# Kernel tuning notes

Measured on AMD Instinct MI355X. Metric: run time of the kernel, lower is better.

The kernel has to match this reference:

```python
import jax, jax.numpy as jnp
import numpy as np

B, S, E = 4, 1024, 1024
H, DH = 16, 64
P = 64  # prompt length
MASKED_BIAS = -10000.0


def setup_inputs() -> dict:
    key = jax.random.key(0)
    ks = jax.random.split(key, 9)
    return {
        "hidden_states": jax.random.normal(ks[0], (B, S, E), jnp.float32),
        "promptKey": jax.random.normal(ks[1], (B, H, P, DH), jnp.float32),
        "promptValue": jax.random.normal(ks[2], (B, H, P, DH), jnp.float32),
        "textualKey": jax.random.normal(ks[3], (B, H, S, DH), jnp.float32),
        "textualValue": jax.random.normal(ks[4], (B, H, S, DH), jnp.float32),
        "promptMask": jnp.ones((B, 1, S, P), jnp.bool_),
        "c_attn_w": jax.random.normal(ks[5], (E, 3 * E), jnp.float32) * 0.02,
        "c_attn_b": jnp.zeros((3 * E,), jnp.float32),
        "c_proj_w": jax.random.normal(ks[6], (E, E), jnp.float32) * 0.02,
        "c_proj_b": jnp.zeros((E,), jnp.float32),
    }


def _split_heads(t):
    # [B, S, E] -> [B, H, S, DH]
    b, s, _ = t.shape
    return t.reshape(b, s, H, DH).transpose(0, 2, 1, 3)


def reference(hidden_states, promptKey, promptValue, textualKey, textualValue,
              promptMask, c_attn_w, c_attn_b, c_proj_w, c_proj_b):
    qkv = hidden_states @ c_attn_w + c_attn_b          # [B,S,3E]
    q, k, v = jnp.split(qkv, 3, axis=-1)
    q, k, v = _split_heads(q), _split_heads(k), _split_heads(v)  # [B,H,S,DH]

    # scores against prompt KV, textual KV, and elementwise self term
    promptW = jnp.einsum("bhsd,bhpd->bhsp", q, promptKey)       # [B,H,S,P]
    textW = jnp.einsum("bhsd,bhtd->bhst", q, textualKey)        # [B,H,S,S]
    selfW = jnp.sum(q * k, axis=-1, keepdims=True)              # [B,H,S,1]
    attn_weights = jnp.concatenate((promptW, textW, selfW), axis=-1)
    attn_weights = attn_weights / jnp.sqrt(jnp.float32(DH))

    # non-residual causal mask: bias[qlen-qlen:qlen, 1:klen+1] -> strictly lower tri
    causal = jnp.tri(S, S, -1, dtype=bool)                      # [S,S]
    self_mask = jnp.ones((S, 1), dtype=bool)
    causal_self = jnp.concatenate((causal, self_mask), axis=-1)[None, None]  # [1,1,S,S+1]
    full_mask = jnp.concatenate(
        (promptMask, jnp.broadcast_to(causal_self, (B, 1, S, S + 1))), axis=-1)
    attn_weights = jnp.where(full_mask, attn_weights, MASKED_BIAS)
    attn_weights = jax.nn.softmax(attn_weights, axis=-1)

    wSelf = attn_weights[..., -1:]                              # [B,H,S,1]
    wRest = attn_weights[..., :-1]                              # [B,H,S,P+S]
    valuePast = jnp.concatenate((promptValue, textualValue), axis=-2)  # [B,H,P+S,DH]
    attn_output = jnp.einsum("bhsk,bhkd->bhsd", wRest, valuePast) + wSelf * v

    # merge heads and output projection
    attn_output = attn_output.transpose(0, 2, 1, 3).reshape(B, S, E)
    return attn_output @ c_proj_w + c_proj_b
```

## Files before the change

### kernel.cpp

```cpp
#include <hip/hip_runtime.h>
#include <hip/hip_bf16.h>
#include <stdint.h>

#define H_ 16
#define DH_ 64
#define S_ 1024
#define B_ 4
#define E_ 1024
#define P_ 64
#define BH_ (B_ * H_)
#define KV_ (P_ + S_)
#define NT_ 17
#define TILE_ELEMS 4096

typedef __attribute__((ext_vector_type(8))) short short8;
typedef __attribute__((ext_vector_type(4))) float floatx4;

#define MFMA_BF16(a, b, c) __builtin_amdgcn_mfma_f32_16x16x32_bf16((a), (b), (c), 0, 0, 0)

__device__ __forceinline__ float bf2f(unsigned short u) {
    union { float f; uint32_t i; } x;
    x.i = ((uint32_t)u) << 16;
    return x.f;
}
__device__ __forceinline__ unsigned short f2bf(float f) {
    uint32_t i = __float_as_uint(f);
    uint32_t r = (i + 0x7fffu + ((i >> 16) & 1u)) >> 16;
    return (unsigned short)r;
}

__device__ __forceinline__ void gl_lds16(const void* g, void* l) {
    __builtin_amdgcn_global_load_lds(
        (const __attribute__((address_space(1))) uint32_t*)g,
        (__attribute__((address_space(3))) uint32_t*)l, 16, 0, 0);
}

#define BARRIER() asm volatile("s_barrier" ::: "memory")
#define WAIT_VM(n) asm volatile("s_waitcnt vmcnt(" #n ")" ::: "memory")

__global__ void prep(const float* __restrict__ hidden, const float* __restrict__ cw,
                     const float* __restrict__ pw, const float* __restrict__ pK,
                     const float* __restrict__ tK, const float* __restrict__ pV,
                     const float* __restrict__ tV, unsigned short* __restrict__ Ah,
                     unsigned short* __restrict__ Wt1, unsigned short* __restrict__ Wt2,
                     unsigned short* __restrict__ Kp, unsigned short* __restrict__ Vp) {
    __shared__ float t[32][33];
    int bid = blockIdx.x, tid = threadIdx.x;
    if (bid < 4096) {
        int i = bid * 256 + tid;
        float4 v = ((const float4*)hidden)[i];
        ushort4 o;
        o.x = f2bf(v.x); o.y = f2bf(v.y); o.z = f2bf(v.z); o.w = f2bf(v.w);
        ((ushort4*)Ah)[i] = o;
    } else if (bid < 8192) {
        const float* in; unsigned short* out; int R, C, bxx, byy;
        if (bid < 7168) { int i = bid - 4096; in = cw; out = Wt1; R = 1024; C = 3072; bxx = i % 96; byy = i / 96; }
        else            { int i = bid - 7168; in = pw; out = Wt2; R = 1024; C = 1024; bxx = i % 32; byy = i / 32; }
        int tx = tid & 31, ty = tid >> 5;
        int c0 = bxx * 32, r0 = byy * 32;
#pragma unroll
        for (int i = 0; i < 4; ++i)
            t[ty + i * 8][tx] = in[(size_t)(r0 + ty + i * 8) * C + c0 + tx];
        __syncthreads();
#pragma unroll
        for (int i = 0; i < 4; ++i)
            out[(size_t)(c0 + ty + i * 8) * R + r0 + tx] = f2bf(t[tx][ty + i * 8]);
    } else {
        int gid0 = (bid - 8192) * 256 + tid;
        int half = gid0 / (BH_ * 8704);
        int gid = gid0 % (BH_ * 8704);
        int bh = gid / 8704, rem = gid % 8704;
        int tt = rem / 512, r2 = rem % 512;
        int f = r2 >> 6, lane = r2 & 63;
        int nt = f >> 1, h = f & 1, quad = lane >> 4, cl = lane & 15;
        unsigned short o[8];
        if (half == 0) {
            int key = tt * 64 + nt * 16 + cl;
            int dh = h * 32 + quad * 8;
            const float* src = (key < P_)
                ? pK + ((size_t)bh * P_ + key) * DH_ + dh
                : tK + ((size_t)bh * S_ + (key - P_)) * DH_ + dh;
#pragma unroll
            for (int u = 0; u < 8; ++u) o[u] = f2bf(src[u]);
            *(int4*)&Kp[(size_t)gid * 8] = *(int4*)o;
        } else {
            int dhn = nt * 16 + cl;
            int kbase = tt * 64 + h * 32 + quad * 8;
            const float* src = (kbase < P_)
                ? pV + ((size_t)bh * P_ + kbase) * DH_ + dhn
                : tV + ((size_t)bh * S_ + (kbase - P_)) * DH_ + dhn;
#pragma unroll
            for (int u = 0; u < 8; ++u) o[u] = f2bf(src[(size_t)u * DH_]);
            *(int4*)&Vp[(size_t)gid * 8] = *(int4*)o;
        }
    }
}

template <int MODE, int TM, int TN, int BK>
__global__ __launch_bounds__(256) void gemm_bt(
    const unsigned short* __restrict__ A, const unsigned short* __restrict__ Bt,
    const float* __restrict__ bias, float* __restrict__ Cout,
    unsigned short* __restrict__ Qo, unsigned short* __restrict__ Ko,
    unsigned short* __restrict__ Vo, int M, int N, int K) {
    constexpr int MI = TM / 32, NI = TN / 32;
    constexpr int NA = TM * BK / 2048;
    constexpr int NB = TN * BK / 2048;
    static_assert(NA + NB == 4, "vmcnt constant assumes 4 loads/tile");
    __shared__ __align__(16) unsigned short lA[2][TM * BK];
    __shared__ __align__(16) unsigned short lB[2][TN * BK];
    int tid = threadIdx.x;
    int wave = tid >> 6, lane = tid & 63, quad = lane >> 4, cl = lane & 15;
    int m0 = blockIdx.y * TM, n0 = blockIdx.x * TN;
    int wm = (wave >> 1) * (TM / 2), wn = (wave & 1) * (TN / 2);
    floatx4 acc[MI][NI];
#pragma unroll
    for (int mi = 0; mi < MI; ++mi)
#pragma unroll
        for (int ni = 0; ni < NI; ++ni) acc[mi][ni] = (floatx4){0.f, 0.f, 0.f, 0.f};

    auto issue = [&](int k0, int buf) {
#pragma unroll
        for (int li = 0; li < NA; ++li) {
            int o = (li * 256 + tid) * 16;
            int hh = o / (TM * 64), rr = (o % (TM * 64)) >> 6, c8 = (o >> 4) & 3;
            gl_lds16(A + (size_t)(m0 + rr) * K + k0 + hh * 32 + c8 * 8,
                     (char*)lA[buf] + o);
        }
#pragma unroll
        for (int li = 0; li < NB; ++li) {
            int o = (li * 256 + tid) * 16;
            int hh = o / (TN * 64), rr = (o % (TN * 64)) >> 6, c8 = (o >> 4) & 3;
            gl_lds16(Bt + (size_t)(n0 + rr) * K + k0 + hh * 32 + c8 * 8,
                     (char*)lB[buf] + o);
        }
    };
    auto compute = [&](int buf) {
#pragma unroll
        for (int kk = 0; kk < BK / 32; ++kk) {
            short8 af[MI], bfr[NI];
#pragma unroll
            for (int mi = 0; mi < MI; ++mi)
                af[mi] = *(const short8*)&lA[buf][kk * TM * 32 + (wm + mi * 16 + cl) * 32 + quad * 8];
#pragma unroll
            for (int ni = 0; ni < NI; ++ni)
                bfr[ni] = *(const short8*)&lB[buf][kk * TN * 32 + (wn + ni * 16 + cl) * 32 + quad * 8];
#pragma unroll
            for (int mi = 0; mi < MI; ++mi)
#pragma unroll
                for (int ni = 0; ni < NI; ++ni)
                    acc[mi][ni] = MFMA_BF16(af[mi], bfr[ni], acc[mi][ni]);
        }
    };

    int nT = K / BK;
    issue(0, 0);
    for (int t = 0; t < nT; ++t) {
        int buf = t & 1;
        if (t + 1 < nT) {
            issue((t + 1) * BK, buf ^ 1);
            WAIT_VM(4);
        } else {
            WAIT_VM(0);
        }
        BARRIER();
        compute(buf);
        BARRIER();
    }

#pragma unroll
    for (int ni = 0; ni < NI; ++ni) {
        int ncol = n0 + wn + ni * 16 + cl;
        float bv = bias[ncol];
#pragma unroll
        for (int mi = 0; mi < MI; ++mi) {
#pragma unroll
            for (int r = 0; r < 4; ++r) {
                int mrow = m0 + wm + mi * 16 + quad * 4 + r;
                float v = acc[mi][ni][r] + bv;
                if (MODE == 0) {
                    Cout[(size_t)mrow * N + ncol] = v;
                } else {
                    int which = ncol >> 10, e = ncol & 1023;
                    int hh = e >> 6, dh = e & 63;
                    int b = mrow >> 10, s = mrow & 1023;
                    size_t idx = ((size_t)(b * H_ + hh) * S_ + s) * DH_ + dh;
                    unsigned short* dst = (which == 0) ? Qo : ((which == 1) ? Ko : Vo);
                    dst[idx] = f2bf(v);
                }
            }
        }
    }
}

__global__ __launch_bounds__(256) void attn_k(
    const unsigned short* __restrict__ Q, const unsigned short* __restrict__ Kc,
    const unsigned short* __restrict__ Vc, const unsigned short* __restrict__ Kp,
    const unsigned short* __restrict__ Vp, unsigned short* __restrict__ Aout) {
    __shared__ __align__(16) unsigned short lP[4][16 * 72];
    int tid = threadIdx.x, wave = tid >> 6, lane = tid & 63;
    int quad = lane >> 4, cl = lane & 15;
    int l = blockIdx.x;
    int p = l >> 6, bh = l & 63;
    int b = bh >> 4, h = bh & 15;
    const unsigned short* Qb = Q + (size_t)bh * S_ * DH_;
    const unsigned short* Kb = Kc + (size_t)bh * S_ * DH_;
    const unsigned short* Vb = Vc + (size_t)bh * S_ * DH_;
    const unsigned short* Kpb = Kp + (size_t)bh * NT_ * TILE_ELEMS;
    const unsigned short* Vpb = Vp + (size_t)bh * NT_ * TILE_ELEMS;
    unsigned short* lp = lP[wave];

    int x1 = p, x2 = 15 - p;
    int qb1 = x1 * 64 + wave * 16, qb2 = x2 * 64 + wave * 16;

    short8 a0_1 = *(const short8*)(Qb + (size_t)(qb1 + cl) * DH_ + quad * 8);
    short8 a1_1 = *(const short8*)(Qb + (size_t)(qb1 + cl) * DH_ + quad * 8 + 32);
    short8 a0_2 = *(const short8*)(Qb + (size_t)(qb2 + cl) * DH_ + quad * 8);
    short8 a1_2 = *(const short8*)(Qb + (size_t)(qb2 + cl) * DH_ + quad * 8 + 32);

    float lsum1[4] = {0.f, 0.f, 0.f, 0.f}, lsum2[4] = {0.f, 0.f, 0.f, 0.f};
    floatx4 O1[4], O2[4];
#pragma unroll
    for (int nt = 0; nt < 4; ++nt) {
        O1[nt] = (floatx4){0.f, 0.f, 0.f, 0.f};
        O2[nt] = (floatx4){0.f, 0.f, 0.f, 0.f};
    }

    int rl = wave * 16 + quad * 4;

    auto do_tile = [&](const unsigned short* Kt, const unsigned short* Vt,
                       short8 a0, short8 a1, floatx4* O, float* lsum, bool diag) {
        floatx4 s[4];
        short8 k0[4], k1[4], v0[4], v1[4];
#pragma unroll
        for (int nt = 0; nt < 4; ++nt) {
            k0[nt] = *(const short8*)&Kt[(nt * 2 + 0) * 512 + lane * 8];
            k1[nt] = *(const short8*)&Kt[(nt * 2 + 1) * 512 + lane * 8];
        }
#pragma unroll
        for (int nt = 0; nt < 4; ++nt) {
            s[nt] = (floatx4){0.f, 0.f, 0.f, 0.f};
            s[nt] = MFMA_BF16(a0, k0[nt], s[nt]);
            s[nt] = MFMA_BF16(a1, k1[nt], s[nt]);
        }
#pragma unroll
        for (int nt = 0; nt < 4; ++nt) {
            v0[nt] = *(const short8*)&Vt[(nt * 2 + 0) * 512 + lane * 8];
            v1[nt] = *(const short8*)&Vt[(nt * 2 + 1) * 512 + lane * 8];
        }
#pragma unroll
        for (int nt = 0; nt < 4; ++nt) {
            int col = nt * 16 + cl;
#pragma unroll
            for (int r = 0; r < 4; ++r) {
                float v = s[nt][r] * 0.125f;
                if (diag && col >= rl + r) v = -10000.0f;
                float pb = __expf(v);
                lsum[r] += pb;
                lp[(quad * 4 + r) * 72 + col] = f2bf(pb);
            }
        }
        asm volatile("s_waitcnt lgkmcnt(0)" ::: "memory");
        short8 p0 = *(const short8*)&lp[cl * 72 + quad * 8];
        short8 p1 = *(const short8*)&lp[cl * 72 + quad * 8 + 32];
#pragma unroll
        for (int nt = 0; nt < 4; ++nt) {
            O[nt] = MFMA_BF16(p0, v0[nt], O[nt]);
            O[nt] = MFMA_BF16(p1, v1[nt], O[nt]);
        }
    };

    int T1 = x1 + 2, Tu = x2 + 2;
    for (int t = 0; t < Tu; ++t) {
        const unsigned short* Kt = Kpb + (size_t)t * TILE_ELEMS;
        const unsigned short* Vt = Vpb + (size_t)t * TILE_ELEMS;
        do_tile(Kt, Vt, a0_2, a1_2, O2, lsum2, t == Tu - 1);
        if (t < T1) do_tile(Kt, Vt, a0_1, a1_1, O1, lsum1, t == T1 - 1);
    }

#pragma unroll
    for (int seg = 0; seg < 2; ++seg) {
        int qb = seg ? qb2 : qb1;
        float* lsum = seg ? lsum2 : lsum1;
        floatx4* O = seg ? O2 : O1;
#pragma unroll
        for (int r = 0; r < 4; ++r) {
            float rs = lsum[r];
            rs += __shfl_xor(rs, 1, 16);
            rs += __shfl_xor(rs, 2, 16);
            rs += __shfl_xor(rs, 4, 16);
            rs += __shfl_xor(rs, 8, 16);
            int row = qb + quad * 4 + r;
            const unsigned short* qp = Qb + (size_t)row * DH_ + cl * 4;
            const unsigned short* kp = Kb + (size_t)row * DH_ + cl * 4;
            float d = 0.f;
#pragma unroll
            for (int u = 0; u < 4; ++u) d += bf2f(qp[u]) * bf2f(kp[u]);
            d += __shfl_xor(d, 1, 16);
            d += __shfl_xor(d, 2, 16);
            d += __shfl_xor(d, 4, 16);
            d += __shfl_xor(d, 8, 16);
            float ps = __expf(d * 0.125f);
            float linv = 1.0f / (rs + ps);
#pragma unroll
            for (int nt = 0; nt < 4; ++nt) {
                float vv = bf2f(Vb[(size_t)row * DH_ + nt * 16 + cl]);
                float o = (O[nt][r] + ps * vv) * linv;
                Aout[((size_t)b * S_ + row) * E_ + h * DH_ + nt * 16 + cl] = f2bf(o);
            }
        }
    }
}

extern "C" void kernel_launch(void* const* d_in, const int* in_sizes, int n_in,
                              void* d_out, int out_size, void* d_ws, size_t ws_size,
                              hipStream_t stream) {
    const float* hidden = (const float*)d_in[0];
    const float* pK = (const float*)d_in[1];
    const float* pV = (const float*)d_in[2];
    const float* tK = (const float*)d_in[3];
    const float* tV = (const float*)d_in[4];
    const float* cw = (const float*)d_in[6];
    const float* cb = (const float*)d_in[7];
    const float* pw = (const float*)d_in[8];
    const float* pb = (const float*)d_in[9];
    float* out = (float*)d_out;

    unsigned short* ws = (unsigned short*)d_ws;
    unsigned short* Wt1 = ws;
    unsigned short* Wt2 = Wt1 + (size_t)3072 * 1024;
    unsigned short* Ah  = Wt2 + (size_t)1024 * 1024;
    unsigned short* Qw  = Ah + (size_t)4096 * 1024;
    unsigned short* Kw  = Qw + (size_t)BH_ * S_ * DH_;
    unsigned short* Vw  = Kw + (size_t)BH_ * S_ * DH_;
    unsigned short* Kp  = Vw + (size_t)BH_ * S_ * DH_;
    unsigned short* Vp  = Kp + (size_t)BH_ * NT_ * TILE_ELEMS;
    unsigned short* At  = Ah;

    prep<<<12544, 256, 0, stream>>>(hidden, cw, pw, pK, tK, pV, tV,
                                    Ah, Wt1, Wt2, Kp, Vp);
    gemm_bt<1, 128, 128, 32><<<dim3(3072 / 128, 4096 / 128), 256, 0, stream>>>(
        Ah, Wt1, cb, nullptr, Qw, Kw, Vw, 4096, 3072, 1024);
    attn_k<<<512, 256, 0, stream>>>(Qw, Kw, Vw, Kp, Vp, At);
    gemm_bt<0, 64, 64, 64><<<dim3(1024 / 64, 4096 / 128 * 2), 256, 0, stream>>>(
        At, Wt2, pb, out, nullptr, nullptr, nullptr, 4096, 1024, 1024);
}
```

Before: 200.9 us.

## Stage attention K/V tiles through LDS, swizzle GEMM LDS, use exp2

The attention kernel now double-buffers each K/V tile into shared memory with async global-to-LDS loads, so all four waves share one global fetch instead of each reading the tile from global memory. The GEMM's LDS layout gets an XOR swizzle on the 16-byte chunk index to cut bank conflicts on the MFMA fragment reads. Softmax exponentials become exp2f with a pre-folded scale, and masked entries are set to zero directly. In exchange the attention kernel uses more shared memory and adds two barriers per tile, which may lower occupancy.

```diff
diff --git a/kernel.cpp b/kernel.cpp
--- a/kernel.cpp
+++ b/kernel.cpp
@@ -17,6 +17,8 @@
 typedef __attribute__((ext_vector_type(4))) float floatx4;
 
 #define MFMA_BF16(a, b, c) __builtin_amdgcn_mfma_f32_16x16x32_bf16((a), (b), (c), 0, 0, 0)
+
+#define EXP_SCALE 0.18033688011112042f
 
 __device__ __forceinline__ float bf2f(unsigned short u) {
     union { float f; uint32_t i; } x;
@@ -112,6 +114,7 @@
     int wave = tid >> 6, lane = tid & 63, quad = lane >> 4, cl = lane & 15;
     int m0 = blockIdx.y * TM, n0 = blockIdx.x * TN;
     int wm = (wave >> 1) * (TM / 2), wn = (wave & 1) * (TN / 2);
+    int cq = quad ^ ((cl >> 1) & 3);
     floatx4 acc[MI][NI];
 #pragma unroll
     for (int mi = 0; mi < MI; ++mi)
@@ -123,14 +126,16 @@
         for (int li = 0; li < NA; ++li) {
             int o = (li * 256 + tid) * 16;
             int hh = o / (TM * 64), rr = (o % (TM * 64)) >> 6, c8 = (o >> 4) & 3;
-            gl_lds16(A + (size_t)(m0 + rr) * K + k0 + hh * 32 + c8 * 8,
+            int q = c8 ^ ((rr >> 1) & 3);
+            gl_lds16(A + (size_t)(m0 + rr) * K + k0 + hh * 32 + q * 8,
                      (char*)lA[buf] + o);
         }
 #pragma unroll
         for (int li = 0; li < NB; ++li) {
             int o = (li * 256 + tid) * 16;
             int hh = o / (TN * 64), rr = (o % (TN * 64)) >> 6, c8 = (o >> 4) & 3;
-            gl_lds16(Bt + (size_t)(n0 + rr) * K + k0 + hh * 32 + c8 * 8,
+            int q = c8 ^ ((rr >> 1) & 3);
+            gl_lds16(Bt + (size_t)(n0 + rr) * K + k0 + hh * 32 + q * 8,
                      (char*)lB[buf] + o);
         }
     };
@@ -140,10 +145,10 @@
             short8 af[MI], bfr[NI];
 #pragma unroll
             for (int mi = 0; mi < MI; ++mi)
-                af[mi] = *(const short8*)&lA[buf][kk * TM * 32 + (wm + mi * 16 + cl) * 32 + quad * 8];
+                af[mi] = *(const short8*)&lA[buf][kk * TM * 32 + (wm + mi * 16 + cl) * 32 + cq * 8];
 #pragma unroll
             for (int ni = 0; ni < NI; ++ni)
-                bfr[ni] = *(const short8*)&lB[buf][kk * TN * 32 + (wn + ni * 16 + cl) * 32 + quad * 8];
+                bfr[ni] = *(const short8*)&lB[buf][kk * TN * 32 + (wn + ni * 16 + cl) * 32 + cq * 8];
 #pragma unroll
             for (int mi = 0; mi < MI; ++mi)
 #pragma unroll
@@ -196,6 +201,8 @@
     const unsigned short* __restrict__ Q, const unsigned short* __restrict__ Kc,
     const unsigned short* __restrict__ Vc, const unsigned short* __restrict__ Kp,
     const unsigned short* __restrict__ Vp, unsigned short* __restrict__ Aout) {
+    __shared__ __align__(16) unsigned short lK[2][TILE_ELEMS];
+    __shared__ __align__(16) unsigned short lV[2][TILE_ELEMS];
     __shared__ __align__(16) unsigned short lP[4][16 * 72];
     int tid = threadIdx.x, wave = tid >> 6, lane = tid & 63;
     int quad = lane >> 4, cl = lane & 15;
@@ -208,6 +215,7 @@
     const unsigned short* Kpb = Kp + (size_t)bh * NT_ * TILE_ELEMS;
     const unsigned short* Vpb = Vp + (size_t)bh * NT_ * TILE_ELEMS;
     unsigned short* lp = lP[wave];
+    int so = wave * 1024 + lane * 16;
 
     int x1 = p, x2 = 15 - p;
     int qb1 = x1 * 64 + wave * 16, qb2 = x2 * 64 + wave * 16;
@@ -227,20 +235,26 @@
 
     int rl = wave * 16 + quad * 4;
 
+    auto issue_tile = [&](int t, int bi) {
+        const char* gK = (const char*)(Kpb + (size_t)t * TILE_ELEMS);
+        const char* gV = (const char*)(Vpb + (size_t)t * TILE_ELEMS);
+        gl_lds16(gK + so, (char*)lK[bi] + so);
+        gl_lds16(gK + 4096 + so, (char*)lK[bi] + 4096 + so);
+        gl_lds16(gV + so, (char*)lV[bi] + so);
+        gl_lds16(gV + 4096 + so, (char*)lV[bi] + 4096 + so);
+    };
+
     auto do_tile = [&](const unsigned short* Kt, const unsigned short* Vt,
                        short8 a0, short8 a1, floatx4* O, float* lsum, bool diag) {
         floatx4 s[4];
-        short8 k0[4], k1[4], v0[4], v1[4];
-#pragma unroll
-        for (int nt = 0; nt < 4; ++nt) {
-            k0[nt] = *(const short8*)&Kt[(nt * 2 + 0) * 512 + lane * 8];
-            k1[nt] = *(const short8*)&Kt[(nt * 2 + 1) * 512 + lane * 8];
-        }
+        short8 v0[4], v1[4];
 #pragma unroll
         for (int nt = 0; nt < 4; ++nt) {
             s[nt] = (floatx4){0.f, 0.f, 0.f, 0.f};
-            s[nt] = MFMA_BF16(a0, k0[nt], s[nt]);
-            s[nt] = MFMA_BF16(a1, k1[nt], s[nt]);
+            short8 k0 = *(const short8*)&Kt[(nt * 2 + 0) * 512 + lane * 8];
+            short8 k1 = *(const short8*)&Kt[(nt * 2 + 1) * 512 + lane * 8];
+            s[nt] = MFMA_BF16(a0, k0, s[nt]);
+            s[nt] = MFMA_BF16(a1, k1, s[nt]);
         }
 #pragma unroll
         for (int nt = 0; nt < 4; ++nt) {
@@ -252,9 +266,8 @@
             int col = nt * 16 + cl;
 #pragma unroll
             for (int r = 0; r < 4; ++r) {
-                float v = s[nt][r] * 0.125f;
-                if (diag && col >= rl + r) v = -10000.0f;
-                float pb = __expf(v);
+                float pb = (diag && col >= rl + r) ? 0.f
+                                                   : exp2f(s[nt][r] * EXP_SCALE);
                 lsum[r] += pb;
                 lp[(quad * 4 + r) * 72 + col] = f2bf(pb);
             }
@@ -270,11 +283,20 @@
     };
 
     int T1 = x1 + 2, Tu = x2 + 2;
+    issue_tile(0, 0);
     for (int t = 0; t < Tu; ++t) {
-        const unsigned short* Kt = Kpb + (size_t)t * TILE_ELEMS;
-        const unsigned short* Vt = Vpb + (size_t)t * TILE_ELEMS;
-        do_tile(Kt, Vt, a0_2, a1_2, O2, lsum2, t == Tu - 1);
-        if (t < T1) do_tile(Kt, Vt, a0_1, a1_1, O1, lsum1, t == T1 - 1);
+        int bi = t & 1;
+        if (t + 1 < Tu) {
+            issue_tile(t + 1, bi ^ 1);
+            WAIT_VM(4);
+        } else {
+            WAIT_VM(0);
+        }
+        BARRIER();
+
+        do_tile(lK[bi], lV[bi], a0_2, a1_2, O2, lsum2, t == Tu - 1);
+        if (t < T1) do_tile(lK[bi], lV[bi], a0_1, a1_1, O1, lsum1, t == T1 - 1);
+        BARRIER();
     }
 
 #pragma unroll
@@ -299,7 +321,7 @@
             d += __shfl_xor(d, 2, 16);
             d += __shfl_xor(d, 4, 16);
             d += __shfl_xor(d, 8, 16);
-            float ps = __expf(d * 0.125f);
+            float ps = exp2f(d * EXP_SCALE);
             float linv = 1.0f / (rs + ps);
 #pragma unroll
             for (int nt = 0; nt < 4; ++nt) {
```

Result: no change. 202.0 us (+0.5%).
